# Kernel optimization log

Measured on AMD Instinct MI355X. Metric: run time of the kernel, lower is better.

Reference implementation:

```python
import jax, jax.numpy as jnp
import numpy as np

DIM = 64
NUM_GRAPHS = 500
N_NODES = 50000
N_EDGES = 100000
PROC_STEPS = 6  # both conv/GRU iterations and Set2Set processing steps


def setup_inputs() -> dict:
    key = jax.random.key(0)
    ks = jax.random.split(key, 32)
    d = DIM
    f = lambda k, shape, s=0.05: jax.random.normal(k, shape, dtype=jnp.float32) * s
    return {
        "x": jax.random.normal(ks[0], (N_NODES, 3), dtype=jnp.float32),
        "edge_index": jax.random.randint(ks[1], (2, N_EDGES), 0, N_NODES),
        "edge_attr": jax.random.uniform(ks[2], (N_EDGES, 7), dtype=jnp.float32),
        "batch": jnp.sort(jax.random.randint(ks[3], (N_NODES,), 0, NUM_GRAPHS)),
        "lin0_w": f(ks[4], (d, 3)), "lin0_b": f(ks[5], (d,)),
        "mlp_w1": f(ks[6], (128, 7)), "mlp_b1": f(ks[7], (128,)),
        "mlp_w2": f(ks[8], (d * d, 128)), "mlp_b2": f(ks[9], (d * d,)),
        "conv_root": f(ks[10], (d, d)), "conv_bias": f(ks[11], (d,)),
        "gru_w_ih": f(ks[12], (3 * d, d)), "gru_w_hh": f(ks[13], (3 * d, d)),
        "gru_b_ih": f(ks[14], (3 * d,)), "gru_b_hh": f(ks[15], (3 * d,)),
        "s2s_w_ih": f(ks[16], (4 * d, 2 * d)), "s2s_w_hh": f(ks[17], (4 * d, d)),
        "s2s_b_ih": f(ks[18], (4 * d,)), "s2s_b_hh": f(ks[19], (4 * d,)),
        "mem_w_ih": f(ks[20], (8 * d, 2 * d)), "mem_w_hh": f(ks[21], (8 * d, 2 * d)),
        "mem_b_ih": f(ks[22], (8 * d,)), "mem_b_hh": f(ks[23], (8 * d,)),
        "lin1_w": f(ks[24], (d, 2 * d)), "lin1_b": f(ks[25], (d,)),
        "lin3_w": f(ks[26], (1, d)), "lin3_b": f(ks[27], (1,)),
    }


def _forward(x, edge_index, edge_attr, batch,
             lin0_w, lin0_b, mlp_w1, mlp_b1, mlp_w2, mlp_b2,
             conv_root, conv_bias,
             gru_w_ih, gru_w_hh, gru_b_ih, gru_b_hh,
             s2s_w_ih, s2s_w_hh, s2s_b_ih, s2s_b_hh,
             mem_w_ih, mem_w_hh, mem_b_ih, mem_b_hh,
             lin1_w, lin1_b, lin3_w, lin3_b):
    d = lin0_w.shape[0]
    n = x.shape[0]
    B = NUM_GRAPHS
    src, dst = edge_index[0], edge_index[1]

    # NNConv edge-conditioned weights (edge_attr is constant across iterations)
    h1 = jax.nn.relu(edge_attr @ mlp_w1.T + mlp_b1)          # [E,128]
    Wmat = (h1 @ mlp_w2.T + mlp_b2).reshape(-1, d, d)        # [E,d_in,d_out]
    deg = jnp.maximum(
        jax.ops.segment_sum(jnp.ones_like(dst, jnp.float32), dst, n), 1.0)

    out = jax.nn.relu(x @ lin0_w.T + lin0_b)                  # [N,d]
    h = out                                                   # GRU hidden, [N,d]
    for _ in range(PROC_STEPS):
        # NNConv: per-edge matmul, mean scatter, root weight + bias
        msg = jnp.einsum('ei,eio->eo', out[src], Wmat)        # [E,d]
        agg = jax.ops.segment_sum(msg, dst, n) / deg[:, None]
        m = jax.nn.relu(agg + out @ conv_root + conv_bias)
        # GRU step (seq len 1)
        gi = m @ gru_w_ih.T + gru_b_ih
        gh = h @ gru_w_hh.T + gru_b_hh
        i_r, i_z, i_n = jnp.split(gi, 3, axis=-1)
        h_r, h_z, h_n = jnp.split(gh, 3, axis=-1)
        r = jax.nn.sigmoid(i_r + h_r)
        z = jax.nn.sigmoid(i_z + h_z)
        nn_ = jnp.tanh(i_n + r * h_n)
        h = (1.0 - z) * nn_ + z * h
        out = h

    # Set2Set pooling (processing_steps = 6)
    hs = jnp.zeros((B, d), dtype=x.dtype)
    cs = jnp.zeros((B, d), dtype=x.dtype)
    q_star = jnp.zeros((B, 2 * d), dtype=x.dtype)
    for _ in range(PROC_STEPS):
        gates = q_star @ s2s_w_ih.T + s2s_b_ih + hs @ s2s_w_hh.T + s2s_b_hh
        ii, ff, gg, oo = jnp.split(gates, 4, axis=-1)
        cs = jax.nn.sigmoid(ff) * cs + jax.nn.sigmoid(ii) * jnp.tanh(gg)
        hs = jax.nn.sigmoid(oo) * jnp.tanh(cs)
        q = hs                                                # [B,d]
        e = jnp.sum(out * q[batch], axis=-1)                  # [N]
        e_max = jax.ops.segment_max(e, batch, B)
        a = jnp.exp(e - e_max[batch])
        a = a / jax.ops.segment_sum(a, batch, B)[batch]       # segment softmax
        r_ = jax.ops.segment_sum(a[:, None] * out, batch, B)  # [B,d]
        q_star = jnp.concatenate([q, r_], axis=-1)            # [B,2d]

    # memory LSTM: seq len 1, zero initial state => h0 @ w_hh == 0
    gates = q_star @ mem_w_ih.T + mem_b_ih + mem_b_hh         # [B,8d]
    ii, ff, gg, oo = jnp.split(gates, 4, axis=-1)
    c = jax.nn.sigmoid(ii) * jnp.tanh(gg)
    hmem = jax.nn.sigmoid(oo) * jnp.tanh(c)

    o1 = jax.nn.relu(hmem @ lin1_w.T + lin1_b)
    v = o1 @ lin3_w.T + lin3_b                                # [B,1]
    return v, hmem[None], c[None]


def reference(x, edge_index, edge_attr, batch,
              lin0_w, lin0_b, mlp_w1, mlp_b1, mlp_w2, mlp_b2,
              conv_root, conv_bias,
              gru_w_ih, gru_w_hh, gru_b_ih, gru_b_hh,
              s2s_w_ih, s2s_w_hh, s2s_b_ih, s2s_b_hh,
              mem_w_ih, mem_w_hh, mem_b_ih, mem_b_hh,
              lin1_w, lin1_b, lin3_w, lin3_b):
    return _forward(x, edge_index, edge_attr, batch,
                    lin0_w, lin0_b, mlp_w1, mlp_b1, mlp_w2, mlp_b2,
                    conv_root, conv_bias,
                    gru_w_ih, gru_w_hh, gru_b_ih, gru_b_hh,
                    s2s_w_ih, s2s_w_hh, s2s_b_ih, s2s_b_hh,
                    mem_w_ih, mem_w_hh, mem_b_ih, mem_b_hh,
                    lin1_w, lin1_b, lin3_w, lin3_b)
```

## Files before the change

kernel.cpp:

```cpp
#include <hip/hip_runtime.h>

#define NN 50000
#define NE 100000
#define NB 500
#define NEP 100096
#define NKF 136
#define CKF 8

typedef _Float16 half2_t __attribute__((ext_vector_type(2)));
typedef _Float16 half8_t __attribute__((ext_vector_type(8)));
typedef float f32x16 __attribute__((ext_vector_type(16)));

union F8U { half8_t v; uint4 u; };

__device__ __forceinline__ float sigm(float x){ return 1.0f/(1.0f + __expf(-x)); }
__device__ __forceinline__ unsigned short f16u(float f){
  _Float16 h = (_Float16)f; return *(unsigned short*)&h;
}


__global__ void k_gstart(const int* __restrict__ batch, int* __restrict__ gst){
  int g = blockIdx.x*blockDim.x + threadIdx.x;
  if (g > NB) return;
  if (g == NB){ gst[g] = NN; return; }
  int lo=0, hi=NN;
  while (lo < hi){ int mid=(lo+hi)>>1; if (batch[mid] < g) lo = mid+1; else hi = mid; }
  gst[g] = lo;
}

__global__ void k_deg(const int* __restrict__ dst, float* __restrict__ deg){
  int e = blockIdx.x*blockDim.x + threadIdx.x;
  if (e < NE) atomicAdd(&deg[dst[e]], 1.0f);
}

__global__ void k_rdeg(float* __restrict__ deg){
  int i = blockIdx.x*blockDim.x + threadIdx.x;
  if (i < NN) deg[i] = 1.0f / fmaxf(deg[i], 1.0f);
}

__global__ void k_h1T(const float* __restrict__ ea, const float* __restrict__ w1,
                      const float* __restrict__ b1, _Float16* __restrict__ h1T){
  int e = blockIdx.x*256 + threadIdx.x;
  int j = blockIdx.y;
  if (e >= NE) return;
  float s;
  if (j == 128){
    s = 1.0f;
  } else {
    const float* a = ea + (size_t)e*7;
    const float* wr = w1 + j*7;
    s = b1[j];
    #pragma unroll
    for (int k=0;k<7;k++) s = fmaf(a[k], wr[k], s);
    s = fmaxf(s, 0.0f);
  }
  h1T[(size_t)j*NEP + e] = (_Float16)s;
}

__global__ void k_lin0(const float* __restrict__ x, const float* __restrict__ w,
                       const float* __restrict__ b, float* __restrict__ hbuf){
  int idx = blockIdx.x*blockDim.x + threadIdx.x;
  if (idx >= NN*64) return;
  int n = idx >> 6, o = idx & 63;
  const float* xr = x + n*3;
  const float* wr = w + o*3;
  float s = b[o] + xr[0]*wr[0] + xr[1]*wr[1] + xr[2]*wr[2];
  hbuf[idx] = fmaxf(s, 0.0f);
}

__global__ void k_prepB(const float* __restrict__ w2, const float* __restrict__ b2,
                        _Float16* __restrict__ B2s){
  int idx = blockIdx.x*blockDim.x + threadIdx.x;
  if (idx >= 129*4096) return;
  int kf = idx >> 12, r = idx & 4095, o = r >> 6, i = r & 63;
  float v = (kf < 128) ? w2[(size_t)(i*64+o)*128 + kf] : b2[i*64+o];
  int byt = (o*128 + i*2) ^ ((o&7)<<4);
  *(unsigned short*)((char*)B2s + (size_t)kf*8192 + byt) = f16u(v);
}

__global__ void k_prepW(const float* __restrict__ root, const float* __restrict__ wih,
                        const float* __restrict__ whh, _Float16* __restrict__ Wg){
  int idx = blockIdx.x*blockDim.x + threadIdx.x;
  if (idx >= 28672) return;
  if (idx < 4096){
    int o = idx >> 6, k = idx & 63;
    int byt = (o*128 + k*2) ^ ((o&7)<<4);
    *(unsigned short*)((char*)Wg + byt) = f16u(root[k*64 + o]);
  } else {
    int x = idx - 4096;
    int o = x >> 7, k = x & 127;
    float v = (k < 64) ? wih[o*64 + k] : whh[o*64 + (k-64)];
    int byt = (o*256 + k*2) ^ ((o&7)<<4);
    *(unsigned short*)((char*)Wg + 8192 + byt) = f16u(v);
  }
}

__global__ __launch_bounds__(256) void k_msgemm2(
    const _Float16* __restrict__ h1T, const _Float16* __restrict__ B2s,
    const float* __restrict__ hbuf, const int* __restrict__ src,
    const int* __restrict__ dst, float* __restrict__ agg){
  __shared__ __align__(16) _Float16 Bsh[CKF*4096];
  __shared__ __align__(16) _Float16 h1sh[CKF*256];
  __shared__ int dst_s[256];
  const int t = threadIdx.x;
  const int lane = t & 63, wv = t >> 6;
  const int hi = lane >> 5, lm = lane & 31;
  const int we = wv >> 1, wo = wv & 1;
  const int o0 = wo * 32;
  const int e0 = blockIdx.x * 256;
  {
    int eg = e0 + t;
    dst_s[t] = (eg < NE) ? dst[eg] : -1;
  }
  half8_t xa[4][4];
  #pragma unroll
  for (int tt=0; tt<4; ++tt){
    int eg = e0 + tt*64 + we*32 + lm;
    int sidx = (eg < NE) ? src[eg] : 0;
    const float4* xr = (const float4*)(hbuf + (size_t)sidx*64);
    #pragma unroll
    for (int q=0;q<4;++q){
      float4 a = xr[q*4 + hi*2];
      float4 b = xr[q*4 + hi*2 + 1];
      half8_t h;
      h[0]=(_Float16)a.x; h[1]=(_Float16)a.y; h[2]=(_Float16)a.z; h[3]=(_Float16)a.w;
      h[4]=(_Float16)b.x; h[5]=(_Float16)b.y; h[6]=(_Float16)b.z; h[7]=(_Float16)b.w;
      xa[tt][q] = h;
    }
  }
  f32x16 acc[4] = {};
  for (int c = 0; c < 17; ++c){
    __syncthreads();
    const char* gB = (const char*)B2s + (size_t)c*65536;
    #pragma unroll 4
    for (int r=0;r<16;++r){
      uint4 u = *(const uint4*)(gB + r*4096 + t*16);
      *(uint4*)((char*)Bsh + r*4096 + t*16) = u;
    }
    {
      int rr = t >> 5, cc = t & 31;
      uint4 u = *(const uint4*)((const char*)h1T + ((size_t)(c*8+rr)*NEP + (size_t)e0)*2 + cc*16);
      *(uint4*)((char*)h1sh + rr*512 + cc*16) = u;
    }
    __syncthreads();
    #pragma unroll
    for (int kf=0; kf<CKF; ++kf){
      _Float16 hv0 = h1sh[kf*256 +       we*32 + lm];
      _Float16 hv1 = h1sh[kf*256 +  64 + we*32 + lm];
      _Float16 hv2 = h1sh[kf*256 + 128 + we*32 + lm];
      _Float16 hv3 = h1sh[kf*256 + 192 + we*32 + lm];
      half8_t b0 = {hv0,hv0,hv0,hv0,hv0,hv0,hv0,hv0};
      half8_t b1 = {hv1,hv1,hv1,hv1,hv1,hv1,hv1,hv1};
      half8_t b2_ = {hv2,hv2,hv2,hv2,hv2,hv2,hv2,hv2};
      half8_t b3 = {hv3,hv3,hv3,hv3,hv3,hv3,hv3,hv3};
      #pragma unroll
      for (int q=0;q<4;++q){
        F8U bf;
        int byt = (((o0+lm)*128 + q*32 + hi*16) ^ ((lm&7)<<4));
        bf.u = *(const uint4*)((const char*)Bsh + kf*8192 + byt);
        acc[0] = __builtin_amdgcn_mfma_f32_32x32x16_f16(xa[0][q]*b0, bf.v, acc[0], 0,0,0);
        acc[1] = __builtin_amdgcn_mfma_f32_32x32x16_f16(xa[1][q]*b1, bf.v, acc[1], 0,0,0);
        acc[2] = __builtin_amdgcn_mfma_f32_32x32x16_f16(xa[2][q]*b2_, bf.v, acc[2], 0,0,0);
        acc[3] = __builtin_amdgcn_mfma_f32_32x32x16_f16(xa[3][q]*b3, bf.v, acc[3], 0,0,0);
      }
    }
  }
  #pragma unroll
  for (int tt=0;tt<4;++tt){
    #pragma unroll
    for (int r=0;r<16;++r){
      int row = (r&3) + 8*(r>>2) + 4*hi;
      int d = dst_s[tt*64 + we*32 + row];
      if (d >= 0) atomicAdd(&agg[(size_t)d*64 + o0 + lm], acc[tt][r]);
    }
  }
}

__global__ __launch_bounds__(256) void k_node2(
    const float* __restrict__ agg, const float* __restrict__ rdeg,
    float* __restrict__ hbuf, const _Float16* __restrict__ Wg,
    const float* __restrict__ cbias, const float* __restrict__ bih,
    const float* __restrict__ bhh){
  __shared__ __align__(16) _Float16 WB[28672];
  __shared__ __align__(16) _Float16 mT[4][2048];
  const int t = threadIdx.x;
  const int lane = t & 63, wv = t >> 6;
  const int hi = lane >> 5, lm = lane & 31;
  #pragma unroll 2
  for (int r=0;r<14;++r){
    uint4 u = *(const uint4*)((const char*)Wg + r*4096 + t*16);
    *(uint4*)((char*)WB + r*4096 + t*16) = u;
  }
  const int n0 = blockIdx.x*128 + wv*32;
  half8_t ah[4];
  {
    int nr = min(n0 + lm, NN-1);
    const float4* hr = (const float4*)(hbuf + (size_t)nr*64);
    #pragma unroll
    for (int q=0;q<4;++q){
      float4 a = hr[q*4 + hi*2];
      float4 b = hr[q*4 + hi*2 + 1];
      half8_t h;
      h[0]=(_Float16)a.x; h[1]=(_Float16)a.y; h[2]=(_Float16)a.z; h[3]=(_Float16)a.w;
      h[4]=(_Float16)b.x; h[5]=(_Float16)b.y; h[6]=(_Float16)b.z; h[7]=(_Float16)b.w;
      ah[q] = h;
    }
  }
  __syncthreads();
  f32x16 am[2] = {};
  #pragma unroll
  for (int q=0;q<4;++q){
    #pragma unroll
    for (int ot=0;ot<2;++ot){
      int o = ot*32 + lm;
      F8U bf;
      bf.u = *(const uint4*)((const char*)WB + ((o*128 + q*32 + hi*16) ^ ((o&7)<<4)));
      am[ot] = __builtin_amdgcn_mfma_f32_32x32x16_f16(ah[q], bf.v, am[ot], 0,0,0);
    }
  }
  #pragma unroll
  for (int ot=0;ot<2;++ot){
    int col = ot*32 + lm;
    float cb = cbias[col];
    #pragma unroll
    for (int r=0;r<16;++r){
      int row = (r&3) + 8*(r>>2) + 4*hi;
      int n = min(n0 + row, NN-1);
      float mv = fmaxf(fmaf(agg[(size_t)n*64 + col], rdeg[n], am[ot][r] + cb), 0.0f);
      *(unsigned short*)((char*)&mT[wv][0] + ((row*128 + col*2) ^ ((row&7)<<4))) = f16u(mv);
    }
  }
  __syncthreads();
  half8_t amf[4];
  #pragma unroll
  for (int q=0;q<4;++q){
    F8U v;
    v.u = *(const uint4*)((const char*)&mT[wv][0] + ((lm*128 + q*32 + hi*16) ^ ((lm&7)<<4)));
    amf[q] = v.v;
  }
  f32x16 aF[4] = {}; f32x16 aIN[2] = {}; f32x16 aHN[2] = {};
  const char* WGp = (const char*)WB + 8192;
  #pragma unroll
  for (int q=0;q<4;++q){
    #pragma unroll
    for (int ot=0;ot<4;++ot){
      int o = ot*32 + lm;
      F8U bf; bf.u = *(const uint4*)(WGp + ((o*256 + q*32 + hi*16) ^ ((o&7)<<4)));
      aF[ot] = __builtin_amdgcn_mfma_f32_32x32x16_f16(amf[q], bf.v, aF[ot], 0,0,0);
    }
    #pragma unroll
    for (int j=0;j<2;++j){
      int o = (4+j)*32 + lm;
      F8U bf; bf.u = *(const uint4*)(WGp + ((o*256 + q*32 + hi*16) ^ ((o&7)<<4)));
      aIN[j] = __builtin_amdgcn_mfma_f32_32x32x16_f16(amf[q], bf.v, aIN[j], 0,0,0);
    }
  }
  #pragma unroll
  for (int q=0;q<4;++q){
    #pragma unroll
    for (int ot=0;ot<4;++ot){
      int o = ot*32 + lm;
      F8U bf; bf.u = *(const uint4*)(WGp + ((o*256 + 128 + q*32 + hi*16) ^ ((o&7)<<4)));
      aF[ot] = __builtin_amdgcn_mfma_f32_32x32x16_f16(ah[q], bf.v, aF[ot], 0,0,0);
    }
    #pragma unroll
    for (int j=0;j<2;++j){
      int o = (4+j)*32 + lm;
      F8U bf; bf.u = *(const uint4*)(WGp + ((o*256 + 128 + q*32 + hi*16) ^ ((o&7)<<4)));
      aHN[j] = __builtin_amdgcn_mfma_f32_32x32x16_f16(ah[q], bf.v, aHN[j], 0,0,0);
    }
  }
  #pragma unroll
  for (int j=0;j<2;++j){
    int col = j*32 + lm;
    float br = bih[col] + bhh[col];
    float bz = bih[64+col] + bhh[64+col];
    float bin = bih[128+col], bhn = bhh[128+col];
    #pragma unroll
    for (int r=0;r<16;++r){
      int row = (r&3) + 8*(r>>2) + 4*hi;
      int n = n0 + row;
      int nc = min(n, NN-1);
      float rg = sigm(aF[j][r] + br);
      float z  = sigm(aF[2+j][r] + bz);
      float nn_ = tanhf(aIN[j][r] + bin + rg*(aHN[j][r] + bhn));
      float hold = hbuf[(size_t)nc*64 + col];
      float hnew = (1.0f - z)*nn_ + z*hold;
      if (n < NN) hbuf[(size_t)n*64 + col] = hnew;
    }
  }
}

__global__ __launch_bounds__(256) void k_s2s(const float* __restrict__ q_star,
    float* __restrict__ hs, float* __restrict__ cs,
    const float* __restrict__ wih, const float* __restrict__ whh,
    const float* __restrict__ bih, const float* __restrict__ bhh){
  const int g = blockIdx.x, t = threadIdx.x;
  __shared__ float qsh[128], hsh[64], gat[256];
  if (t < 128) qsh[t] = q_star[g*128 + t];
  if (t >= 128 && t < 192) hsh[t-128] = hs[g*64 + (t-128)];
  __syncthreads();
  float s = bih[t] + bhh[t];
  const float* wr = wih + (size_t)t*128;
  #pragma unroll 4
  for (int k=0;k<128;k++) s = fmaf(qsh[k], wr[k], s);
  const float* hr = whh + (size_t)t*64;
  #pragma unroll 4
  for (int k=0;k<64;k++) s = fmaf(hsh[k], hr[k], s);
  gat[t] = s;
  __syncthreads();
  if (t < 64){
    float ii = gat[t], ff = gat[64+t], gg = gat[128+t], oo = gat[192+t];
    float c = sigm(ff)*cs[g*64+t] + sigm(ii)*tanhf(gg);
    float hn = sigm(oo)*tanhf(c);
    cs[g*64+t] = c; hs[g*64+t] = hn;
  }
}

__global__ __launch_bounds__(256) void k_attn(const float* __restrict__ hbuf,
    const float* __restrict__ hs, const int* __restrict__ gst,
    float* __restrict__ ebuf, float* __restrict__ q_star){
  const int g = blockIdx.x;
  const int start = gst[g], end = gst[g+1];
  const int t = threadIdx.x;
  const int lane = t & 63, wv = t >> 6;
  __shared__ float qs[64];
  __shared__ float red[256];
  __shared__ float rpart[4][64];
  if (t < 64) qs[t] = hs[g*64 + t];
  __syncthreads();
  float lmax = -1e30f;
  for (int n = start + t; n < end; n += 256){
    const float4* row = reinterpret_cast<const float4*>(hbuf + (size_t)n*64);
    float s = 0.f;
    #pragma unroll
    for (int k=0;k<16;k++){
      float4 v = row[k];
      s += v.x*qs[4*k] + v.y*qs[4*k+1] + v.z*qs[4*k+2] + v.w*qs[4*k+3];
    }
    ebuf[n] = s;
    lmax = fmaxf(lmax, s);
  }
  red[t] = lmax; __syncthreads();
  for (int off=128; off>0; off>>=1){ if (t<off) red[t] = fmaxf(red[t], red[t+off]); __syncthreads(); }
  const float gmax = red[0]; __syncthreads();
  float lsum = 0.f;
  for (int n = start + t; n < end; n += 256){
    float a = __expf(ebuf[n] - gmax);
    ebuf[n] = a;
    lsum += a;
  }
  red[t] = lsum; __syncthreads();
  for (int off=128; off>0; off>>=1){ if (t<off) red[t] += red[t+off]; __syncthreads(); }
  const float inv = (red[0] > 0.f) ? 1.0f/red[0] : 0.f;
  float racc = 0.f;
  for (int n = start + wv; n < end; n += 4)
    racc = fmaf(ebuf[n], hbuf[(size_t)n*64 + lane], racc);
  rpart[wv][lane] = racc;
  __syncthreads();
  if (t < 64){
    float r = (rpart[0][t] + rpart[1][t] + rpart[2][t] + rpart[3][t]) * inv;
    q_star[g*128 + t] = qs[t];
    q_star[g*128 + 64 + t] = r;
  }
}

__global__ __launch_bounds__(256) void k_final(const float* __restrict__ q_star,
    const float* __restrict__ mwih, const float* __restrict__ mbih,
    const float* __restrict__ mbhh, const float* __restrict__ l1w,
    const float* __restrict__ l1b, const float* __restrict__ l3w,
    const float* __restrict__ l3b, float* __restrict__ out){
  const int g = blockIdx.x, t = threadIdx.x;
  __shared__ float qsh[128], gat[512], hm[128], o1[64];
  if (t < 128) qsh[t] = q_star[g*128 + t];
  __syncthreads();
  for (int r = t; r < 512; r += 256){
    float s = mbih[r] + mbhh[r];
    const float* wr = mwih + (size_t)r*128;
    #pragma unroll 4
    for (int k=0;k<128;k++) s = fmaf(qsh[k], wr[k], s);
    gat[r] = s;
  }
  __syncthreads();
  if (t < 128){
    float c = sigm(gat[t]) * tanhf(gat[256+t]);
    float hmem = sigm(gat[384+t]) * tanhf(c);
    hm[t] = hmem;
    out[500 + g*128 + t] = hmem;
    out[64500 + g*128 + t] = c;
  }
  __syncthreads();
  if (t < 64){
    float s = l1b[t];
    const float* wr = l1w + (size_t)t*128;
    #pragma unroll 4
    for (int k=0;k<128;k++) s = fmaf(hm[k], wr[k], s);
    o1[t] = fmaxf(s, 0.f);
  }
  __syncthreads();
  if (t == 0){
    float v = l3b[0];
    for (int k=0;k<64;k++) v = fmaf(o1[k], l3w[k], v);
    out[g] = v;
  }
}

extern "C" void kernel_launch(void* const* d_in, const int* in_sizes, int n_in,
                              void* d_out, int out_size, void* d_ws, size_t ws_size,
                              hipStream_t stream){
  (void)in_sizes; (void)n_in;
  const float* x     = (const float*)d_in[0];
  const int*   eidx  = (const int*)d_in[1];
  const float* eattr = (const float*)d_in[2];
  const int*   batch = (const int*)d_in[3];
  const float* lin0w = (const float*)d_in[4];
  const float* lin0b = (const float*)d_in[5];
  const float* mw1   = (const float*)d_in[6];
  const float* mb1   = (const float*)d_in[7];
  const float* mw2   = (const float*)d_in[8];
  const float* mb2   = (const float*)d_in[9];
  const float* convr = (const float*)d_in[10];
  const float* convb = (const float*)d_in[11];
  const float* gwih  = (const float*)d_in[12];
  const float* gwhh  = (const float*)d_in[13];
  const float* gbih  = (const float*)d_in[14];
  const float* gbhh  = (const float*)d_in[15];
  const float* swih  = (const float*)d_in[16];
  const float* swhh  = (const float*)d_in[17];
  const float* sbih  = (const float*)d_in[18];
  const float* sbhh  = (const float*)d_in[19];
  const float* mwih  = (const float*)d_in[20];
  const float* mbih  = (const float*)d_in[22];
  const float* mbhh  = (const float*)d_in[23];
  const float* l1w   = (const float*)d_in[24];
  const float* l1b   = (const float*)d_in[25];
  const float* l3w   = (const float*)d_in[26];
  const float* l3b   = (const float*)d_in[27];
  float* out = (float*)d_out;
  const int* src = eidx;
  const int* dstp = eidx + NE;

  size_t off = 0;
  auto take = [&](size_t bytes)->void*{
    void* p = (void*)((char*)d_ws + off);
    off = (off + bytes + 255) & ~(size_t)255;
    return p;
  };
  _Float16* h1T = (_Float16*)take((size_t)NKF*NEP*2);
  _Float16* B2s = (_Float16*)take((size_t)NKF*8192);
  _Float16* Wg  = (_Float16*)take((size_t)28672*2);
  float* hbuf = (float*)take((size_t)NN*64*4);
  float* agg  = (float*)take((size_t)NN*64*4);
  float* deg  = (float*)take((size_t)NN*4);
  float* ebuf = (float*)take((size_t)NN*4);
  int*   gst  = (int*)take((size_t)(NB+1)*4);
  float* qst  = (float*)take((size_t)NB*128*4);
  float* hs   = (float*)take((size_t)NB*64*4);
  float* cs   = (float*)take((size_t)NB*64*4);

  if (off > ws_size){
    hipMemsetAsync(d_out, 0, (size_t)out_size*4, stream);
    return;
  }

  hipMemsetAsync(h1T, 0, (size_t)NKF*NEP*2, stream);
  hipMemsetAsync(deg, 0, (size_t)NN*4, stream);
  k_gstart<<<4, 128, 0, stream>>>(batch, gst);
  k_deg<<<(NE+255)/256, 256, 0, stream>>>(dstp, deg);
  k_rdeg<<<(NN+255)/256, 256, 0, stream>>>(deg);
  k_h1T<<<dim3((NE+255)/256, 129), 256, 0, stream>>>(eattr, mw1, mb1, h1T);
  k_lin0<<<NN*64/256, 256, 0, stream>>>(x, lin0w, lin0b, hbuf);
  k_prepB<<<(129*4096+255)/256, 256, 0, stream>>>(mw2, mb2, B2s);
  k_prepW<<<(28672+255)/256, 256, 0, stream>>>(convr, gwih, gwhh, Wg);

  for (int step = 0; step < 6; ++step){
    hipMemsetAsync(agg, 0, (size_t)NN*64*4, stream);
    k_msgemm2<<<NEP/256, 256, 0, stream>>>(h1T, B2s, hbuf, src, dstp, agg);
    k_node2<<<(NN+127)/128, 256, 0, stream>>>(agg, deg, hbuf, Wg, convb, gbih, gbhh);
  }

  hipMemsetAsync(qst, 0, (size_t)NB*128*4, stream);
  hipMemsetAsync(hs, 0, (size_t)NB*64*4, stream);
  hipMemsetAsync(cs, 0, (size_t)NB*64*4, stream);
  for (int it = 0; it < 6; ++it){
    k_s2s<<<NB, 256, 0, stream>>>(qst, hs, cs, swih, swhh, sbih, sbhh);
    k_attn<<<NB, 256, 0, stream>>>(hbuf, hs, gst, ebuf, qst);
  }
  k_final<<<NB, 256, 0, stream>>>(qst, mwih, mbih, mbhh, l1w, l1b, l3w, l3b, out);
}
```

Measured before the change: 1.219 ms.

## Fuse Set2Set iterations and readout into one kernel; halve GEMM k-chunk

Merges the six Set2Set LSTM and attention iterations plus the final readout into one per-graph kernel that keeps LSTM state and q_star in shared memory. This removes many small launches and the global state buffers with their memsets. Separately, the message GEMM stages its weights in chunks of 4 k-rows instead of 8, which means twice as many chunk iterations and barriers. It also zero-pads the staged weight tensor to 136 rows so padded rows are defined.

```diff
diff --git a/kernel.cpp b/kernel.cpp
--- a/kernel.cpp
+++ b/kernel.cpp
@@ -5,7 +5,7 @@
 #define NB 500
 #define NEP 100096
 #define NKF 136
-#define CKF 8
+#define CKF 4
 
 typedef _Float16 half2_t __attribute__((ext_vector_type(2)));
 typedef _Float16 half8_t __attribute__((ext_vector_type(8)));
@@ -71,9 +71,9 @@
 __global__ void k_prepB(const float* __restrict__ w2, const float* __restrict__ b2,
                         _Float16* __restrict__ B2s){
   int idx = blockIdx.x*blockDim.x + threadIdx.x;
-  if (idx >= 129*4096) return;
+  if (idx >= NKF*4096) return;
   int kf = idx >> 12, r = idx & 4095, o = r >> 6, i = r & 63;
-  float v = (kf < 128) ? w2[(size_t)(i*64+o)*128 + kf] : b2[i*64+o];
+  float v = (kf < 128) ? w2[(size_t)(i*64+o)*128 + kf] : (kf == 128 ? b2[i*64+o] : 0.0f);
   int byt = (o*128 + i*2) ^ ((o&7)<<4);
   *(unsigned short*)((char*)B2s + (size_t)kf*8192 + byt) = f16u(v);
 }
@@ -129,17 +129,17 @@
     }
   }
   f32x16 acc[4] = {};
-  for (int c = 0; c < 17; ++c){
-    __syncthreads();
-    const char* gB = (const char*)B2s + (size_t)c*65536;
+  for (int c = 0; c < NKF/CKF; ++c){
+    __syncthreads();
+    const char* gB = (const char*)B2s + (size_t)c*(CKF*8192);
     #pragma unroll 4
-    for (int r=0;r<16;++r){
+    for (int r=0;r<8;++r){
       uint4 u = *(const uint4*)(gB + r*4096 + t*16);
       *(uint4*)((char*)Bsh + r*4096 + t*16) = u;
     }
-    {
+    if (t < 128){
       int rr = t >> 5, cc = t & 31;
-      uint4 u = *(const uint4*)((const char*)h1T + ((size_t)(c*8+rr)*NEP + (size_t)e0)*2 + cc*16);
+      uint4 u = *(const uint4*)((const char*)h1T + ((size_t)(c*CKF+rr)*NEP + (size_t)e0)*2 + cc*16);
       *(uint4*)((char*)h1sh + rr*512 + cc*16) = u;
     }
     __syncthreads();
@@ -291,88 +291,80 @@
   }
 }
 
-__global__ __launch_bounds__(256) void k_s2s(const float* __restrict__ q_star,
-    float* __restrict__ hs, float* __restrict__ cs,
-    const float* __restrict__ wih, const float* __restrict__ whh,
-    const float* __restrict__ bih, const float* __restrict__ bhh){
-  const int g = blockIdx.x, t = threadIdx.x;
-  __shared__ float qsh[128], hsh[64], gat[256];
-  if (t < 128) qsh[t] = q_star[g*128 + t];
-  if (t >= 128 && t < 192) hsh[t-128] = hs[g*64 + (t-128)];
-  __syncthreads();
-  float s = bih[t] + bhh[t];
-  const float* wr = wih + (size_t)t*128;
-  #pragma unroll 4
-  for (int k=0;k<128;k++) s = fmaf(qsh[k], wr[k], s);
-  const float* hr = whh + (size_t)t*64;
-  #pragma unroll 4
-  for (int k=0;k<64;k++) s = fmaf(hsh[k], hr[k], s);
-  gat[t] = s;
-  __syncthreads();
-  if (t < 64){
-    float ii = gat[t], ff = gat[64+t], gg = gat[128+t], oo = gat[192+t];
-    float c = sigm(ff)*cs[g*64+t] + sigm(ii)*tanhf(gg);
-    float hn = sigm(oo)*tanhf(c);
-    cs[g*64+t] = c; hs[g*64+t] = hn;
-  }
-}
-
-__global__ __launch_bounds__(256) void k_attn(const float* __restrict__ hbuf,
-    const float* __restrict__ hs, const int* __restrict__ gst,
-    float* __restrict__ ebuf, float* __restrict__ q_star){
-  const int g = blockIdx.x;
-  const int start = gst[g], end = gst[g+1];
-  const int t = threadIdx.x;
-  const int lane = t & 63, wv = t >> 6;
-  __shared__ float qs[64];
-  __shared__ float red[256];
-  __shared__ float rpart[4][64];
-  if (t < 64) qs[t] = hs[g*64 + t];
-  __syncthreads();
-  float lmax = -1e30f;
-  for (int n = start + t; n < end; n += 256){
-    const float4* row = reinterpret_cast<const float4*>(hbuf + (size_t)n*64);
-    float s = 0.f;
-    #pragma unroll
-    for (int k=0;k<16;k++){
-      float4 v = row[k];
-      s += v.x*qs[4*k] + v.y*qs[4*k+1] + v.z*qs[4*k+2] + v.w*qs[4*k+3];
-    }
-    ebuf[n] = s;
-    lmax = fmaxf(lmax, s);
-  }
-  red[t] = lmax; __syncthreads();
-  for (int off=128; off>0; off>>=1){ if (t<off) red[t] = fmaxf(red[t], red[t+off]); __syncthreads(); }
-  const float gmax = red[0]; __syncthreads();
-  float lsum = 0.f;
-  for (int n = start + t; n < end; n += 256){
-    float a = __expf(ebuf[n] - gmax);
-    ebuf[n] = a;
-    lsum += a;
-  }
-  red[t] = lsum; __syncthreads();
-  for (int off=128; off>0; off>>=1){ if (t<off) red[t] += red[t+off]; __syncthreads(); }
-  const float inv = (red[0] > 0.f) ? 1.0f/red[0] : 0.f;
-  float racc = 0.f;
-  for (int n = start + wv; n < end; n += 4)
-    racc = fmaf(ebuf[n], hbuf[(size_t)n*64 + lane], racc);
-  rpart[wv][lane] = racc;
-  __syncthreads();
-  if (t < 64){
-    float r = (rpart[0][t] + rpart[1][t] + rpart[2][t] + rpart[3][t]) * inv;
-    q_star[g*128 + t] = qs[t];
-    q_star[g*128 + 64 + t] = r;
-  }
-}
-
-__global__ __launch_bounds__(256) void k_final(const float* __restrict__ q_star,
+__global__ __launch_bounds__(256) void k_tail(
+    const float* __restrict__ hbuf, const int* __restrict__ gst,
+    float* __restrict__ ebuf,
+    const float* __restrict__ swih, const float* __restrict__ swhh,
+    const float* __restrict__ sbih, const float* __restrict__ sbhh,
     const float* __restrict__ mwih, const float* __restrict__ mbih,
     const float* __restrict__ mbhh, const float* __restrict__ l1w,
     const float* __restrict__ l1b, const float* __restrict__ l3w,
     const float* __restrict__ l3b, float* __restrict__ out){
   const int g = blockIdx.x, t = threadIdx.x;
-  __shared__ float qsh[128], gat[512], hm[128], o1[64];
-  if (t < 128) qsh[t] = q_star[g*128 + t];
+  const int start = gst[g], end = gst[g+1];
+  const int lane = t & 63, wv = t >> 6;
+  __shared__ float qsh[128];
+  __shared__ float hsh[64], csh[64];
+  __shared__ float gat[512];
+  __shared__ float red[256];
+  __shared__ float rpart[4][64];
+  __shared__ float hm[128], o1[64];
+  if (t < 128) qsh[t] = 0.f;
+  if (t < 64){ hsh[t] = 0.f; csh[t] = 0.f; }
+  for (int it = 0; it < 6; ++it){
+    __syncthreads();
+    {
+      float s = sbih[t] + sbhh[t];
+      const float* wr = swih + (size_t)t*128;
+      #pragma unroll 4
+      for (int k=0;k<128;k++) s = fmaf(qsh[k], wr[k], s);
+      const float* hr = swhh + (size_t)t*64;
+      #pragma unroll 4
+      for (int k=0;k<64;k++) s = fmaf(hsh[k], hr[k], s);
+      gat[t] = s;
+    }
+    __syncthreads();
+    if (t < 64){
+      float ii = gat[t], ff = gat[64+t], gg = gat[128+t], oo = gat[192+t];
+      float c = sigm(ff)*csh[t] + sigm(ii)*tanhf(gg);
+      csh[t] = c;
+      hsh[t] = sigm(oo)*tanhf(c);
+    }
+    __syncthreads();
+    float lmax = -1e30f;
+    for (int n = start + t; n < end; n += 256){
+      const float4* row = (const float4*)(hbuf + (size_t)n*64);
+      float s = 0.f;
+      #pragma unroll
+      for (int k=0;k<16;k++){
+        float4 v = row[k];
+        s += v.x*hsh[4*k] + v.y*hsh[4*k+1] + v.z*hsh[4*k+2] + v.w*hsh[4*k+3];
+      }
+      ebuf[n] = s;
+      lmax = fmaxf(lmax, s);
+    }
+    red[t] = lmax; __syncthreads();
+    for (int o2=128; o2>0; o2>>=1){ if (t<o2) red[t] = fmaxf(red[t], red[t+o2]); __syncthreads(); }
+    const float gmax = red[0]; __syncthreads();
+    float lsum = 0.f;
+    for (int n = start + t; n < end; n += 256){
+      float a = __expf(ebuf[n] - gmax);
+      ebuf[n] = a;
+      lsum += a;
+    }
+    red[t] = lsum; __syncthreads();
+    for (int o2=128; o2>0; o2>>=1){ if (t<o2) red[t] += red[t+o2]; __syncthreads(); }
+    const float inv = (red[0] > 0.f) ? 1.0f/red[0] : 0.f;
+    float racc = 0.f;
+    for (int n = start + wv; n < end; n += 4)
+      racc = fmaf(ebuf[n], hbuf[(size_t)n*64 + lane], racc);
+    rpart[wv][lane] = racc;
+    __syncthreads();
+    if (t < 64){
+      qsh[t] = hsh[t];
+      qsh[64+t] = (rpart[0][t] + rpart[1][t] + rpart[2][t] + rpart[3][t]) * inv;
+    }
+  }
   __syncthreads();
   for (int r = t; r < 512; r += 256){
     float s = mbih[r] + mbhh[r];
@@ -454,9 +446,6 @@
   float* deg  = (float*)take((size_t)NN*4);
   float* ebuf = (float*)take((size_t)NN*4);
   int*   gst  = (int*)take((size_t)(NB+1)*4);
-  float* qst  = (float*)take((size_t)NB*128*4);
-  float* hs   = (float*)take((size_t)NB*64*4);
-  float* cs   = (float*)take((size_t)NB*64*4);
 
   if (off > ws_size){
     hipMemsetAsync(d_out, 0, (size_t)out_size*4, stream);
@@ -470,7 +459,7 @@
   k_rdeg<<<(NN+255)/256, 256, 0, stream>>>(deg);
   k_h1T<<<dim3((NE+255)/256, 129), 256, 0, stream>>>(eattr, mw1, mb1, h1T);
   k_lin0<<<NN*64/256, 256, 0, stream>>>(x, lin0w, lin0b, hbuf);
-  k_prepB<<<(129*4096+255)/256, 256, 0, stream>>>(mw2, mb2, B2s);
+  k_prepB<<<(NKF*4096+255)/256, 256, 0, stream>>>(mw2, mb2, B2s);
   k_prepW<<<(28672+255)/256, 256, 0, stream>>>(convr, gwih, gwhh, Wg);
 
   for (int step = 0; step < 6; ++step){
@@ -479,12 +468,6 @@
     k_node2<<<(NN+127)/128, 256, 0, stream>>>(agg, deg, hbuf, Wg, convb, gbih, gbhh);
   }
 
-  hipMemsetAsync(qst, 0, (size_t)NB*128*4, stream);
-  hipMemsetAsync(hs, 0, (size_t)NB*64*4, stream);
-  hipMemsetAsync(cs, 0, (size_t)NB*64*4, stream);
-  for (int it = 0; it < 6; ++it){
-    k_s2s<<<NB, 256, 0, stream>>>(qst, hs, cs, swih, swhh, sbih, sbhh);
-    k_attn<<<NB, 256, 0, stream>>>(hbuf, hs, gst, ebuf, qst);
-  }
-  k_final<<<NB, 256, 0, stream>>>(qst, mwih, mbih, mbhh, l1w, l1b, l3w, l3b, out);
-}
+  k_tail<<<NB, 256, 0, stream>>>(hbuf, gst, ebuf, swih, swhh, sbih, sbhh,
+                                 mwih, mbih, mbhh, l1w, l1b, l3w, l3b, out);
+}
```

After: 1.235 ms. About the same (+1.3%).
